# Optimization experiments

Measured on AMD Instinct MI355X. Metric: run time of the kernel, lower is better.

## Reference

```python
import jax, jax.numpy as jnp
import numpy as np

N, E, D, H, L = 100000, 1600000, 128, 64, 3
BN_EPS = 1e-5


def setup_inputs() -> dict:
    key = jax.random.key(0)
    ks = iter(jax.random.split(key, 32))
    r = lambda shape, s=0.05: jax.random.normal(next(ks), shape, dtype=jnp.float32) * s
    inp = {
        "x": jax.random.normal(next(ks), (N, D), dtype=jnp.float32),
        "edge_index": jax.random.randint(next(ks), (2, E), 0, N, dtype=jnp.int64),
        "fa_W1": r((D, H)), "fa_b1": jnp.zeros((H,), jnp.float32),
        "fa_W2": r((H, D)), "fa_b2": jnp.zeros((D,), jnp.float32),
        "proj_W": r((D, H)), "proj_b": jnp.zeros((H,), jnp.float32),
        "gat_W": r((L, H, H)), "gat_asrc": r((L, H)), "gat_adst": r((L, H)),
        "gat_b": jnp.zeros((L, H), jnp.float32),
        "bn_gamma": jnp.ones((L, H), jnp.float32), "bn_beta": jnp.zeros((L, H), jnp.float32),
        "bn_mean": jnp.zeros((L, H), jnp.float32), "bn_var": jnp.ones((L, H), jnp.float32),
        "se_W1": r((3, H // 2)), "se_b1": jnp.zeros((H // 2,), jnp.float32),
        "se_W2": r((H // 2, H)), "se_b2": jnp.zeros((H,), jnp.float32),
        "out_W1": r((2 * H, H)), "out_b1": jnp.zeros((H,), jnp.float32),
        "out_W2": r((H, H // 2)), "out_b2": jnp.zeros((H // 2,), jnp.float32),
        "out_W3": r((H // 2, 1)), "out_b3": jnp.zeros((1,), jnp.float32),
    }
    return inp


def _gat_layer(h, src, dst, n, W, a_src, a_dst, b):
    # PyG GATConv (heads=1, self-loops already appended to src/dst).
    z = h @ W                              # [N,H]
    e = jax.nn.leaky_relu((z @ a_src)[src] + (z @ a_dst)[dst], 0.2)  # [Etot]
    m = jax.ops.segment_max(e, dst, num_segments=n)
    m = jnp.where(jnp.isfinite(m), m, 0.0)
    ex = jnp.exp(e - m[dst])
    denom = jax.ops.segment_sum(ex, dst, num_segments=n)
    alpha = ex / denom[dst]
    return jax.ops.segment_sum(z[src] * alpha[:, None], dst, num_segments=n) + b


def _structural(edge_index, n, dtype):
    src, dst = edge_index[0], edge_index[1]
    deg = jax.ops.segment_sum(jnp.ones(src.shape, dtype), src, num_segments=n)
    norm_deg = deg / jnp.maximum(deg.max(), 1.0)
    infl_sum = jax.ops.segment_sum(deg[dst], src, num_segments=n)
    infl = jnp.where(deg > 0, infl_sum / jnp.maximum(deg, 1.0), 0.0)
    infl = infl / jnp.maximum(infl.max(), 1e-12)
    return jnp.stack([norm_deg, jnp.zeros_like(deg), infl], axis=1)  # [N,3]


def reference(x, edge_index, fa_W1, fa_b1, fa_W2, fa_b2, proj_W, proj_b,
              gat_W, gat_asrc, gat_adst, gat_b, bn_gamma, bn_beta, bn_mean, bn_var,
              se_W1, se_b1, se_W2, se_b2, out_W1, out_b1, out_W2, out_b2, out_W3, out_b3):
    n = x.shape[0]
    # feature attention
    fw = jax.nn.sigmoid(jnp.maximum(x @ fa_W1 + fa_b1, 0.0) @ fa_W2 + fa_b2)
    h = (x * fw) @ proj_W + proj_b
    # self loops for GAT
    loop = jnp.arange(n, dtype=edge_index.dtype)
    src = jnp.concatenate([edge_index[0], loop])
    dst = jnp.concatenate([edge_index[1], loop])
    for l in range(L):
        h = _gat_layer(h, src, dst, n, gat_W[l], gat_asrc[l], gat_adst[l], gat_b[l])
        h = (h - bn_mean[l]) * jax.lax.rsqrt(bn_var[l] + BN_EPS) * bn_gamma[l] + bn_beta[l]
        h = jnp.maximum(h, 0.0)  # eval mode: dropout is identity
    sf = _structural(edge_index, n, h.dtype)
    se = jnp.maximum(sf @ se_W1 + se_b1, 0.0) @ se_W2 + se_b2
    h = jnp.concatenate([h, se], axis=1)  # [N, 2H]
    o = jnp.maximum(h @ out_W1 + out_b1, 0.0)
    o = jnp.maximum(o @ out_W2 + out_b2, 0.0)
    return jax.nn.sigmoid(o @ out_W3 + out_b3)
```

## Files before the change

### kernel.cpp

```cpp
#include <hip/hip_runtime.h>


typedef unsigned int uint;
typedef unsigned short ushort;
typedef __attribute__((ext_vector_type(8))) short bf16x8;
typedef __attribute__((ext_vector_type(4))) float f32x4;

__device__ __forceinline__ uint f2bf(float a) {
    uint u = __float_as_uint(a);
    return (u + 0x7fffu + ((u >> 16) & 1u)) >> 16;
}
__device__ __forceinline__ float bflo(uint p) { return __uint_as_float(p << 16); }
__device__ __forceinline__ float bfhi(uint p) { return __uint_as_float(p & 0xffff0000u); }
__device__ __forceinline__ float b2f16(ushort u) { return __uint_as_float((uint)u << 16); }

__device__ __forceinline__ void packOne(const float* W, int C, int KS,
                                        ushort* dst, int o) {
    int j = o & 7, lane = (o >> 3) & 63, f = o >> 9;
    int ks = f % KS, ct = f / KS;
    int row = 32 * ks + 8 * (lane >> 4) + j;
    int col = ct * 16 + (lane & 15);
    dst[o] = (ushort)f2bf(W[row * C + col]);
}

__global__ void k_pack(const float* __restrict__ faW1, const float* __restrict__ faW2,
                       const float* __restrict__ projW, const float* __restrict__ gatW,
                       const float* __restrict__ oW1, const float* __restrict__ oW2,
                       ushort* __restrict__ pA, ushort* __restrict__ pB,
                       ushort* __restrict__ pC, ushort* __restrict__ pG,
                       ushort* __restrict__ pO1u, ushort* __restrict__ pOW2) {
    int i = blockIdx.x * blockDim.x + threadIdx.x;
    if (i < 8192) packOne(faW1, 64, 4, pA, i);
    else if (i < 16384) packOne(faW2, 128, 2, pB, i - 8192);
    else if (i < 24576) packOne(projW, 64, 4, pC, i - 16384);
    else if (i < 36864) {
        int o = i - 24576; int l = o >> 12;
        packOne(gatW + l * 4096, 64, 2, pG + l * 4096, o & 4095);
    } else if (i < 40960) packOne(oW1, 64, 2, pO1u, i - 36864);
    else if (i < 43008) packOne(oW2, 32, 2, pOW2, i - 40960);
}

__global__ void __launch_bounds__(256)
k_fused1(const float* __restrict__ x,
         const ushort* __restrict__ pA, const float* __restrict__ fab1,
         const ushort* __restrict__ pB, const float* __restrict__ fab2,
         const ushort* __restrict__ pC, const float* __restrict__ projb,
         float* __restrict__ hbuf, int N,
         const int* __restrict__ ei, int E,
         float* __restrict__ deg, int* __restrict__ cursor, int* __restrict__ esrc,
         const float* __restrict__ seW2, const float* __restrict__ seb2,
         const float* __restrict__ oW1, const float* __restrict__ ob1,
         float* __restrict__ M2, float* __restrict__ b2f, ushort* __restrict__ pM2f,
         int gMlp, int gEdge) {
    __shared__ ushort S[4][16][136];
    int bid = blockIdx.x;
    if (bid < gMlp) {
        int wave = threadIdx.x >> 6, lane = threadIdx.x & 63;
        int qg = lane >> 4, lr = lane & 15;
        int n0w = (bid * 4 + wave) * 16;
        int nr = n0w + lr; if (nr >= N) nr = N - 1;
        const float* xr = x + (size_t)nr * 128;
        ushort (*T)[136] = S[wave];
        const bf16x8* fA = reinterpret_cast<const bf16x8*>(pA);
        const bf16x8* fB = reinterpret_cast<const bf16x8*>(pB);
        const bf16x8* fC = reinterpret_cast<const bf16x8*>(pC);

        bf16x8 afr[4];
#pragma unroll
        for (int ks = 0; ks < 4; ++ks) {
            const float* p = xr + 32 * ks + 8 * qg;
            float4 v0 = *reinterpret_cast<const float4*>(p);
            float4 v1 = *reinterpret_cast<const float4*>(p + 4);
            bf16x8 a;
            a[0] = (short)f2bf(v0.x); a[1] = (short)f2bf(v0.y);
            a[2] = (short)f2bf(v0.z); a[3] = (short)f2bf(v0.w);
            a[4] = (short)f2bf(v1.x); a[5] = (short)f2bf(v1.y);
            a[6] = (short)f2bf(v1.z); a[7] = (short)f2bf(v1.w);
            afr[ks] = a;
        }
        {
            f32x4 acc[4] = {{0,0,0,0},{0,0,0,0},{0,0,0,0},{0,0,0,0}};
#pragma unroll
            for (int ct = 0; ct < 4; ++ct)
#pragma unroll
                for (int ks = 0; ks < 4; ++ks)
                    acc[ct] = __builtin_amdgcn_mfma_f32_16x16x32_bf16(
                        afr[ks], fA[(ct * 4 + ks) * 64 + lane], acc[ct], 0, 0, 0);
#pragma unroll
            for (int ct = 0; ct < 4; ++ct) {
                float b1v = fab1[ct * 16 + lr];
#pragma unroll
                for (int r = 0; r < 4; ++r)
                    T[qg * 4 + r][ct * 16 + lr] =
                        (ushort)f2bf(fmaxf(acc[ct][r] + b1v, 0.f));
            }
        }
        __syncthreads();

        bf16x8 bfr[2];
#pragma unroll
        for (int ks = 0; ks < 2; ++ks)
            bfr[ks] = *reinterpret_cast<const bf16x8*>(&T[lr][32 * ks + 8 * qg]);
        __syncthreads();
        {
            f32x4 acc[8] = {{0,0,0,0},{0,0,0,0},{0,0,0,0},{0,0,0,0},
                            {0,0,0,0},{0,0,0,0},{0,0,0,0},{0,0,0,0}};
#pragma unroll
            for (int ct = 0; ct < 8; ++ct)
#pragma unroll
                for (int ks = 0; ks < 2; ++ks)
                    acc[ct] = __builtin_amdgcn_mfma_f32_16x16x32_bf16(
                        bfr[ks], fB[(ct * 2 + ks) * 64 + lane], acc[ct], 0, 0, 0);
#pragma unroll
            for (int ct = 0; ct < 8; ++ct) {
                float b2v = fab2[ct * 16 + lr];
#pragma unroll
                for (int r = 0; r < 4; ++r)
                    T[qg * 4 + r][ct * 16 + lr] = (ushort)f2bf(acc[ct][r] + b2v);
            }
        }
        __syncthreads();

        bf16x8 cfr[4];
#pragma unroll
        for (int ks = 0; ks < 4; ++ks) {
            const ushort* pf = &T[lr][32 * ks + 8 * qg];
            const float* px = xr + 32 * ks + 8 * qg;
            float4 x0 = *reinterpret_cast<const float4*>(px);
            float4 x1 = *reinterpret_cast<const float4*>(px + 4);
            bf16x8 a;
            a[0] = (short)f2bf(x0.x / (1.f + __expf(-b2f16(pf[0]))));
            a[1] = (short)f2bf(x0.y / (1.f + __expf(-b2f16(pf[1]))));
            a[2] = (short)f2bf(x0.z / (1.f + __expf(-b2f16(pf[2]))));
            a[3] = (short)f2bf(x0.w / (1.f + __expf(-b2f16(pf[3]))));
            a[4] = (short)f2bf(x1.x / (1.f + __expf(-b2f16(pf[4]))));
            a[5] = (short)f2bf(x1.y / (1.f + __expf(-b2f16(pf[5]))));
            a[6] = (short)f2bf(x1.z / (1.f + __expf(-b2f16(pf[6]))));
            a[7] = (short)f2bf(x1.w / (1.f + __expf(-b2f16(pf[7]))));
            cfr[ks] = a;
        }
        {
            f32x4 acc[4] = {{0,0,0,0},{0,0,0,0},{0,0,0,0},{0,0,0,0}};
#pragma unroll
            for (int ct = 0; ct < 4; ++ct)
#pragma unroll
                for (int ks = 0; ks < 4; ++ks)
                    acc[ct] = __builtin_amdgcn_mfma_f32_16x16x32_bf16(
                        cfr[ks], fC[(ct * 4 + ks) * 64 + lane], acc[ct], 0, 0, 0);
#pragma unroll
            for (int r = 0; r < 4; ++r) {
                int n = n0w + qg * 4 + r;
                if (n < N) {
#pragma unroll
                    for (int ct = 0; ct < 4; ++ct)
                        hbuf[(size_t)n * 64 + ct * 16 + lr] =
                            acc[ct][r] + projb[ct * 16 + lr];
                    if (lr == 0) esrc[(size_t)n * 64] = n;
                }
            }
        }
    } else if (bid < gMlp + gEdge) {
        int e = (bid - gMlp) * blockDim.x + threadIdx.x;
        if (e < E) {
            int s = ei[e], d = ei[E + e];
            atomicAdd(&deg[s], 1.f);
            int p = atomicAdd(&cursor[d], 1);
            esrc[(size_t)d * 64 + 1 + p] = s;
        }
    } else {
        int tid = threadIdx.x;
        for (int o = tid; o < 32 * 64; o += 256) {
            int k = o >> 6, j = o & 63;
            float s = 0.f;
            for (int i = 0; i < 64; ++i)
                s = fmaf(seW2[k * 64 + i], oW1[(64 + i) * 64 + j], s);
            M2[o] = s;
        }
        for (int j = tid; j < 64; j += 256) {
            float s = ob1[j];
            for (int i = 0; i < 64; ++i)
                s = fmaf(seb2[i], oW1[(64 + i) * 64 + j], s);
            b2f[j] = s;
        }
        __syncthreads();
        for (int o = tid; o < 2048; o += 256)
            packOne(M2, 64, 1, pM2f, o);
    }
}

__global__ __attribute__((amdgpu_waves_per_eu(4, 4))) void __launch_bounds__(256)
k_z(const float* __restrict__ hbuf, const ushort* __restrict__ pWz,
    const float* __restrict__ asrc, const float* __restrict__ adst,
    uint* __restrict__ zbuf, float* __restrict__ es, float* __restrict__ ed,
    const int* __restrict__ ei, int E,
    const float* __restrict__ deg, float* __restrict__ inflsum,
    float* __restrict__ inflv, unsigned* __restrict__ scal,
    int N, int gZ, int riderMode) {
    int bid = blockIdx.x;
    if (bid >= gZ) {
        if (riderMode == 1) {
            int e = (bid - gZ) * blockDim.x + threadIdx.x;
            if (e < E) atomicAdd(&inflsum[ei[e]], deg[ei[E + e]]);
        } else {
            int idx = (bid - gZ) * blockDim.x + threadIdx.x;
            float dv = 0.f, iv = 0.f;
            if (idx < N) {
                dv = deg[idx];
                iv = dv > 0.f ? inflsum[idx] / dv : 0.f;
                inflv[idx] = iv;
            }
            float dm = dv, im = iv;
#pragma unroll
            for (int off = 32; off; off >>= 1) {
                dm = fmaxf(dm, __shfl_xor(dm, off, 64));
                im = fmaxf(im, __shfl_xor(im, off, 64));
            }
            if ((threadIdx.x & 63) == 0) {
                atomicMax(scal + 0, __float_as_uint(dm));
                atomicMax(scal + 1, __float_as_uint(im));
            }
        }
        return;
    }
    __shared__ float zt[4][16][68];
    int wave = threadIdx.x >> 6, lane = threadIdx.x & 63;
    int qg = lane >> 4, lr = lane & 15;
    int n0w = (bid * 4 + wave) * 16;
    int nr = n0w + lr; if (nr >= N) nr = N - 1;

    bf16x8 afr[2];
#pragma unroll
    for (int k2 = 0; k2 < 2; ++k2) {
        const float* hp = hbuf + (size_t)nr * 64 + k2 * 32 + qg * 8;
        float4 h0 = *reinterpret_cast<const float4*>(hp);
        float4 h1 = *reinterpret_cast<const float4*>(hp + 4);
        bf16x8 a;
        a[0] = (short)f2bf(h0.x); a[1] = (short)f2bf(h0.y);
        a[2] = (short)f2bf(h0.z); a[3] = (short)f2bf(h0.w);
        a[4] = (short)f2bf(h1.x); a[5] = (short)f2bf(h1.y);
        a[6] = (short)f2bf(h1.z); a[7] = (short)f2bf(h1.w);
        afr[k2] = a;
    }

    const bf16x8* pw = reinterpret_cast<const bf16x8*>(pWz);
    f32x4 acc0 = {0,0,0,0}, acc1 = {0,0,0,0}, acc2 = {0,0,0,0}, acc3 = {0,0,0,0};
#pragma unroll
    for (int k2 = 0; k2 < 2; ++k2) {
        acc0 = __builtin_amdgcn_mfma_f32_16x16x32_bf16(afr[k2], pw[(0 * 2 + k2) * 64 + lane], acc0, 0, 0, 0);
        acc1 = __builtin_amdgcn_mfma_f32_16x16x32_bf16(afr[k2], pw[(1 * 2 + k2) * 64 + lane], acc1, 0, 0, 0);
        acc2 = __builtin_amdgcn_mfma_f32_16x16x32_bf16(afr[k2], pw[(2 * 2 + k2) * 64 + lane], acc2, 0, 0, 0);
        acc3 = __builtin_amdgcn_mfma_f32_16x16x32_bf16(afr[k2], pw[(3 * 2 + k2) * 64 + lane], acc3, 0, 0, 0);
    }

    float (*Z)[68] = zt[wave];
#pragma unroll
    for (int r = 0; r < 4; ++r) {
        Z[qg * 4 + r][0 * 16 + lr] = acc0[r];
        Z[qg * 4 + r][1 * 16 + lr] = acc1[r];
        Z[qg * 4 + r][2 * 16 + lr] = acc2[r];
        Z[qg * 4 + r][3 * 16 + lr] = acc3[r];
    }
    __syncthreads();

    float zr[16];
    const float* zrow = &Z[lr][qg * 16];
#pragma unroll
    for (int q4 = 0; q4 < 4; ++q4) {
        float4 v = *reinterpret_cast<const float4*>(zrow + q4 * 4);
        zr[q4 * 4] = v.x; zr[q4 * 4 + 1] = v.y; zr[q4 * 4 + 2] = v.z; zr[q4 * 4 + 3] = v.w;
    }
    float pe = 0.f, pd = 0.f;
#pragma unroll
    for (int j = 0; j < 16; ++j) {
        pe = fmaf(zr[j], asrc[qg * 16 + j], pe);
        pd = fmaf(zr[j], adst[qg * 16 + j], pd);
    }
    pe += __shfl_xor(pe, 16, 64); pe += __shfl_xor(pe, 32, 64);
    pd += __shfl_xor(pd, 16, 64); pd += __shfl_xor(pd, 32, 64);

    int n = n0w + lr;
    if (n < N) {
        uint4 u0, u1;
        u0.x = f2bf(zr[0]) | (f2bf(zr[1]) << 16);
        u0.y = f2bf(zr[2]) | (f2bf(zr[3]) << 16);
        u0.z = f2bf(zr[4]) | (f2bf(zr[5]) << 16);
        u0.w = f2bf(zr[6]) | (f2bf(zr[7]) << 16);
        u1.x = f2bf(zr[8]) | (f2bf(zr[9]) << 16);
        u1.y = f2bf(zr[10]) | (f2bf(zr[11]) << 16);
        u1.z = f2bf(zr[12]) | (f2bf(zr[13]) << 16);
        u1.w = f2bf(zr[14]) | (f2bf(zr[15]) << 16);
        uint* zr8 = zbuf + (size_t)n * 32 + qg * 8;
        *reinterpret_cast<uint4*>(zr8) = u0;
        *reinterpret_cast<uint4*>(zr8 + 4) = u1;
        if (qg == 0) { es[n] = pe; ed[n] = pd; }
    }
}

__global__ void k_agg(const int* __restrict__ cursor,
                      const int* __restrict__ esrc,
                      const float* __restrict__ es, const float* __restrict__ ed,
                      const uint* __restrict__ zb,
                      const float* __restrict__ b, const float* __restrict__ g,
                      const float* __restrict__ bta, const float* __restrict__ mean,
                      const float* __restrict__ var,
                      float* __restrict__ hbuf, int N) {
    int wid  = (blockIdx.x * blockDim.x + threadIdx.x) >> 6;
    int lane = threadIdx.x & 63;
    if (wid >= N) return;
    size_t row0 = (size_t)wid * 64;
    int c    = cursor[wid] + 1;
    float edn = ed[wid];
    int lq = lane & 15, q = lane >> 4;

    int   sreg = 0;
    float exv  = 0.f;
    if (lane < c) {
        sreg = esrc[row0 + lane];
        float e = es[sreg] + edn;
        e = e >= 0.f ? e : 0.2f * e;
        exv = __expf(e);
    }
    float ssum = exv;
#pragma unroll
    for (int off = 32; off; off >>= 1) ssum += __shfl_xor(ssum, off, 64);

    float a0 = 0.f, a1 = 0.f, a2 = 0.f, a3 = 0.f;
    for (int e = q; e < c; e += 4) {
        int   se = __shfl(sreg, e, 64);
        float we = __shfl(exv, e, 64);
        uint2 p = *reinterpret_cast<const uint2*>(zb + (size_t)se * 32 + lq * 2);
        a0 = fmaf(bflo(p.x), we, a0);
        a1 = fmaf(bfhi(p.x), we, a1);
        a2 = fmaf(bflo(p.y), we, a2);
        a3 = fmaf(bfhi(p.y), we, a3);
    }
    a0 += __shfl_xor(a0, 16, 64); a0 += __shfl_xor(a0, 32, 64);
    a1 += __shfl_xor(a1, 16, 64); a1 += __shfl_xor(a1, 32, 64);
    a2 += __shfl_xor(a2, 16, 64); a2 += __shfl_xor(a2, 32, 64);
    a3 += __shfl_xor(a3, 16, 64); a3 += __shfl_xor(a3, 32, 64);

    if (q == 0) {
        float inv = 1.f / ssum;
        float4 bb = reinterpret_cast<const float4*>(b)[lq];
        float4 gg = reinterpret_cast<const float4*>(g)[lq];
        float4 tt = reinterpret_cast<const float4*>(bta)[lq];
        float4 mm = reinterpret_cast<const float4*>(mean)[lq];
        float4 vv = reinterpret_cast<const float4*>(var)[lq];
        float v0 = (a0 * inv + bb.x - mm.x) * (gg.x * rsqrtf(vv.x + 1e-5f)) + tt.x;
        float v1 = (a1 * inv + bb.y - mm.y) * (gg.y * rsqrtf(vv.y + 1e-5f)) + tt.y;
        float v2 = (a2 * inv + bb.z - mm.z) * (gg.z * rsqrtf(vv.z + 1e-5f)) + tt.z;
        float v3 = (a3 * inv + bb.w - mm.w) * (gg.w * rsqrtf(vv.w + 1e-5f)) + tt.w;
        reinterpret_cast<float4*>(hbuf + (size_t)wid * 64)[lq] =
            make_float4(fmaxf(v0, 0.f), fmaxf(v1, 0.f), fmaxf(v2, 0.f), fmaxf(v3, 0.f));
    }
}

__global__ void __launch_bounds__(256)
k_final(const float* __restrict__ hbuf, const float* __restrict__ deg,
        const float* __restrict__ inflv, const unsigned* __restrict__ scal,
        const float* __restrict__ seW1, const float* __restrict__ seb1,
        const ushort* __restrict__ pM2f, const float* __restrict__ b2f,
        const ushort* __restrict__ pO1u, const ushort* __restrict__ pOW2,
        const float* __restrict__ ob2,
        const float* __restrict__ oW3, const float* __restrict__ ob3,
        float* __restrict__ out, int N) {
    __shared__ ushort S[4][16][136];
    int wave = threadIdx.x >> 6, lane = threadIdx.x & 63;
    int qg = lane >> 4, lr = lane & 15;
    int n0w = (blockIdx.x * 4 + wave) * 16;
    int nr = n0w + lr; if (nr >= N) nr = N - 1;
    ushort (*T)[136] = S[wave];

    float degmax  = fmaxf(__uint_as_float(scal[0]), 1.0f);
    float inflmax = fmaxf(__uint_as_float(scal[1]), 1e-12f);
    float nd = deg[nr] / degmax;
    float fl = inflv[nr] / inflmax;

    bf16x8 a0, a1, a2;
#pragma unroll
    for (int ks = 0; ks < 2; ++ks) {
        const float* hp = hbuf + (size_t)nr * 64 + 32 * ks + 8 * qg;
        float4 h0 = *reinterpret_cast<const float4*>(hp);
        float4 h1 = *reinterpret_cast<const float4*>(hp + 4);
        bf16x8 a;
        a[0] = (short)f2bf(h0.x); a[1] = (short)f2bf(h0.y);
        a[2] = (short)f2bf(h0.z); a[3] = (short)f2bf(h0.w);
        a[4] = (short)f2bf(h1.x); a[5] = (short)f2bf(h1.y);
        a[6] = (short)f2bf(h1.z); a[7] = (short)f2bf(h1.w);
        if (ks == 0) a0 = a; else a1 = a;
    }
#pragma unroll
    for (int j = 0; j < 8; ++j) {
        int k = 8 * qg + j;
        float hid = fmaxf(fmaf(nd, seW1[k], fmaf(fl, seW1[64 + k], seb1[k])), 0.f);
        a2[j] = (short)f2bf(hid);
    }

    const bf16x8* fO1 = reinterpret_cast<const bf16x8*>(pO1u);
    const bf16x8* fM2 = reinterpret_cast<const bf16x8*>(pM2f);
    const bf16x8* fW2 = reinterpret_cast<const bf16x8*>(pOW2);

    {
        f32x4 acc[4] = {{0,0,0,0},{0,0,0,0},{0,0,0,0},{0,0,0,0}};
#pragma unroll
        for (int ct = 0; ct < 4; ++ct) {
            acc[ct] = __builtin_amdgcn_mfma_f32_16x16x32_bf16(a0, fO1[(ct * 2 + 0) * 64 + lane], acc[ct], 0, 0, 0);
            acc[ct] = __builtin_amdgcn_mfma_f32_16x16x32_bf16(a1, fO1[(ct * 2 + 1) * 64 + lane], acc[ct], 0, 0, 0);
            acc[ct] = __builtin_amdgcn_mfma_f32_16x16x32_bf16(a2, fM2[ct * 64 + lane], acc[ct], 0, 0, 0);
        }
#pragma unroll
        for (int ct = 0; ct < 4; ++ct) {
            float bv = b2f[ct * 16 + lr];
#pragma unroll
            for (int r = 0; r < 4; ++r)
                T[qg * 4 + r][ct * 16 + lr] =
                    (ushort)f2bf(fmaxf(acc[ct][r] + bv, 0.f));
        }
    }
    __syncthreads();

    bf16x8 b0 = *reinterpret_cast<const bf16x8*>(&T[lr][8 * qg]);
    bf16x8 b1 = *reinterpret_cast<const bf16x8*>(&T[lr][32 + 8 * qg]);
    f32x4 o2a = {0,0,0,0}, o2b = {0,0,0,0};
    o2a = __builtin_amdgcn_mfma_f32_16x16x32_bf16(b0, fW2[0 * 64 + lane], o2a, 0, 0, 0);
    o2a = __builtin_amdgcn_mfma_f32_16x16x32_bf16(b1, fW2[1 * 64 + lane], o2a, 0, 0, 0);
    o2b = __builtin_amdgcn_mfma_f32_16x16x32_bf16(b0, fW2[2 * 64 + lane], o2b, 0, 0, 0);
    o2b = __builtin_amdgcn_mfma_f32_16x16x32_bf16(b1, fW2[3 * 64 + lane], o2b, 0, 0, 0);

    float w3a = oW3[lr], w3b = oW3[16 + lr];
    float oba = ob2[lr], obb = ob2[16 + lr];
    float part[4];
#pragma unroll
    for (int r = 0; r < 4; ++r)
        part[r] = fmaxf(o2a[r] + oba, 0.f) * w3a + fmaxf(o2b[r] + obb, 0.f) * w3b;
#pragma unroll
    for (int off = 1; off < 16; off <<= 1) {
#pragma unroll
        for (int r = 0; r < 4; ++r) part[r] += __shfl_xor(part[r], off, 64);
    }
    if (lr == 0) {
        float b3 = ob3[0];
#pragma unroll
        for (int r = 0; r < 4; ++r) {
            int n = n0w + qg * 4 + r;
            if (n < N) out[n] = 1.f / (1.f + __expf(-(part[r] + b3)));
        }
    }
}

extern "C" void kernel_launch(void* const* d_in, const int* in_sizes, int n_in,
                              void* d_out, int out_size, void* d_ws, size_t ws_size,
                              hipStream_t stream) {
    const float* x     = (const float*)d_in[0];
    const int*   ei    = (const int*)d_in[1];
    const float* faW1  = (const float*)d_in[2];
    const float* fab1  = (const float*)d_in[3];
    const float* faW2  = (const float*)d_in[4];
    const float* fab2  = (const float*)d_in[5];
    const float* projW = (const float*)d_in[6];
    const float* projb = (const float*)d_in[7];
    const float* gatW  = (const float*)d_in[8];
    const float* gatAs = (const float*)d_in[9];
    const float* gatAd = (const float*)d_in[10];
    const float* gatB  = (const float*)d_in[11];
    const float* bnG   = (const float*)d_in[12];
    const float* bnB   = (const float*)d_in[13];
    const float* bnM   = (const float*)d_in[14];
    const float* bnV   = (const float*)d_in[15];
    const float* seW1  = (const float*)d_in[16];
    const float* seb1  = (const float*)d_in[17];
    const float* seW2  = (const float*)d_in[18];
    const float* seb2  = (const float*)d_in[19];
    const float* oW1   = (const float*)d_in[20];
    const float* ob1   = (const float*)d_in[21];
    const float* oW2   = (const float*)d_in[22];
    const float* ob2   = (const float*)d_in[23];
    const float* oW3   = (const float*)d_in[24];
    const float* ob3   = (const float*)d_in[25];
    float* out = (float*)d_out;

    const int N = in_sizes[0] / 128;
    const int E = in_sizes[1] / 2;

    float* ws      = (float*)d_ws;
    float* hbuf    = ws;
    uint*  zbuf    = (uint*)(hbuf + (size_t)N * 64);
    float* es      = (float*)(zbuf + (size_t)N * 32);
    float* ed      = es + N;
    float* deg     = ed + N;
    float* inflsum = deg + N;
    unsigned* scal = (unsigned*)(inflsum + N);
    int* cursor    = (int*)(scal + 8);
    float* inflv   = (float*)(cursor + N);
    int* esrc      = (int*)(inflv + N);
    float* M2      = (float*)(esrc + (size_t)N * 64);
    float* b2f     = M2 + 32 * 64;
    ushort* pA   = (ushort*)(b2f + 64);
    ushort* pB   = pA + 8192;
    ushort* pC   = pB + 8192;
    ushort* pWz  = pC + 8192;
    ushort* pO1u = pWz + 3 * 4096;
    ushort* pOW2 = pO1u + 4096;
    ushort* pM2f = pOW2 + 2048;

    dim3 blk(256);
    int gN    = (N + 255) / 256;
    int gE    = (E + 255) / 256;
    int gM    = (N + 63) / 64;
    int blkNW = (N * 64 + 255) / 256;

    hipMemsetAsync(deg, 0, ((size_t)3 * N + 8) * sizeof(float), stream);

    k_pack<<<168, blk, 0, stream>>>(faW1, faW2, projW, gatW, oW1, oW2,
                                    pA, pB, pC, pWz, pO1u, pOW2);

    k_fused1<<<gM + gE + 1, blk, 0, stream>>>(x, pA, fab1, pB, fab2, pC, projb,
                                              hbuf, N, ei, E, deg, cursor, esrc,
                                              seW2, seb2, oW1, ob1, M2, b2f, pM2f,
                                              gM, gE);

    for (int l = 0; l < 3; ++l) {
        int extra = (l == 0) ? gE : (l == 1 ? gN : 0);
        int mode  = (l == 0) ? 1  : (l == 1 ? 2  : 0);
        k_z<<<gM + extra, blk, 0, stream>>>(hbuf, pWz + l * 4096, gatAs + l * 64,
                                            gatAd + l * 64, zbuf, es, ed,
                                            ei, E, deg, inflsum, inflv, scal,
                                            N, gM, mode);
        k_agg<<<blkNW, blk, 0, stream>>>(cursor, esrc, es, ed, zbuf,
                                         gatB + l * 64, bnG + l * 64, bnB + l * 64,
                                         bnM + l * 64, bnV + l * 64, hbuf, N);
    }

    k_final<<<gM, blk, 0, stream>>>(hbuf, deg, inflv, scal, seW1, seb1,
                                    pM2f, b2f, pO1u, pOW2, ob2, oW3, ob3, out, N);
}
```

Measured before the change: 517.1 us.

## Fuse layer-0 GAT projection into input MLP kernel and move influence rider

The first GAT layer's z = h@W plus its attention logits es/ed are now computed directly in the feature-attention/projection kernel, with the projected h staged through shared memory as bf16. This removes one k_z launch and the fp32 hbuf write and read round-trip for layer 0. The edge-influence atomic rider moves from k_z into the layer-0 k_agg launch, and the later k_z calls are shifted to prepare layers 1 and 2. In exchange, h is rounded to bf16 before the GAT matmul, and extra __syncthreads calls are added inside a block whose waves otherwise work independently.

```diff
diff --git a/kernel.cpp b/kernel.cpp
--- a/kernel.cpp
+++ b/kernel.cpp
@@ -45,7 +45,10 @@
          const ushort* __restrict__ pA, const float* __restrict__ fab1,
          const ushort* __restrict__ pB, const float* __restrict__ fab2,
          const ushort* __restrict__ pC, const float* __restrict__ projb,
-         float* __restrict__ hbuf, int N,
+         const ushort* __restrict__ pWz0,
+         const float* __restrict__ asrc, const float* __restrict__ adst,
+         uint* __restrict__ zbuf, float* __restrict__ es, float* __restrict__ ed,
+         int N,
          const int* __restrict__ ei, int E,
          float* __restrict__ deg, int* __restrict__ cursor, int* __restrict__ esrc,
          const float* __restrict__ seW2, const float* __restrict__ seb2,
@@ -64,6 +67,7 @@
         const bf16x8* fA = reinterpret_cast<const bf16x8*>(pA);
         const bf16x8* fB = reinterpret_cast<const bf16x8*>(pB);
         const bf16x8* fC = reinterpret_cast<const bf16x8*>(pC);
+        const bf16x8* fZ = reinterpret_cast<const bf16x8*>(pWz0);
 
         bf16x8 afr[4];
 #pragma unroll
@@ -139,6 +143,7 @@
             a[7] = (short)f2bf(x1.w / (1.f + __expf(-b2f16(pf[7]))));
             cfr[ks] = a;
         }
+        __syncthreads();
         {
             f32x4 acc[4] = {{0,0,0,0},{0,0,0,0},{0,0,0,0},{0,0,0,0}};
 #pragma unroll
@@ -148,15 +153,64 @@
                     acc[ct] = __builtin_amdgcn_mfma_f32_16x16x32_bf16(
                         cfr[ks], fC[(ct * 4 + ks) * 64 + lane], acc[ct], 0, 0, 0);
 #pragma unroll
-            for (int r = 0; r < 4; ++r) {
-                int n = n0w + qg * 4 + r;
-                if (n < N) {
-#pragma unroll
-                    for (int ct = 0; ct < 4; ++ct)
-                        hbuf[(size_t)n * 64 + ct * 16 + lr] =
-                            acc[ct][r] + projb[ct * 16 + lr];
-                    if (lr == 0) esrc[(size_t)n * 64] = n;
-                }
+            for (int ct = 0; ct < 4; ++ct) {
+                float pbv = projb[ct * 16 + lr];
+#pragma unroll
+                for (int r = 0; r < 4; ++r)
+                    T[qg * 4 + r][ct * 16 + lr] = (ushort)f2bf(acc[ct][r] + pbv);
+            }
+        }
+        __syncthreads();
+
+        bf16x8 hfr[2];
+#pragma unroll
+        for (int ks = 0; ks < 2; ++ks)
+            hfr[ks] = *reinterpret_cast<const bf16x8*>(&T[lr][32 * ks + 8 * qg]);
+        __syncthreads();
+        {
+            f32x4 zacc[4] = {{0,0,0,0},{0,0,0,0},{0,0,0,0},{0,0,0,0}};
+#pragma unroll
+            for (int ct = 0; ct < 4; ++ct)
+#pragma unroll
+                for (int ks = 0; ks < 2; ++ks)
+                    zacc[ct] = __builtin_amdgcn_mfma_f32_16x16x32_bf16(
+                        hfr[ks], fZ[(ct * 2 + ks) * 64 + lane], zacc[ct], 0, 0, 0);
+#pragma unroll
+            for (int ct = 0; ct < 4; ++ct)
+#pragma unroll
+                for (int r = 0; r < 4; ++r)
+                    T[qg * 4 + r][ct * 16 + lr] = (ushort)f2bf(zacc[ct][r]);
+        }
+        __syncthreads();
+        {
+            bf16x8 z0 = *reinterpret_cast<const bf16x8*>(&T[lr][qg * 16]);
+            bf16x8 z1 = *reinterpret_cast<const bf16x8*>(&T[lr][qg * 16 + 8]);
+            float pe = 0.f, pd = 0.f;
+#pragma unroll
+            for (int j = 0; j < 8; ++j) {
+                float va = b2f16((ushort)z0[j]), vb = b2f16((ushort)z1[j]);
+                pe = fmaf(va, asrc[qg * 16 + j], pe);
+                pe = fmaf(vb, asrc[qg * 16 + 8 + j], pe);
+                pd = fmaf(va, adst[qg * 16 + j], pd);
+                pd = fmaf(vb, adst[qg * 16 + 8 + j], pd);
+            }
+            pe += __shfl_xor(pe, 16, 64); pe += __shfl_xor(pe, 32, 64);
+            pd += __shfl_xor(pd, 16, 64); pd += __shfl_xor(pd, 32, 64);
+            int n = n0w + lr;
+            if (n < N) {
+                uint4 u0, u1;
+                u0.x = (ushort)z0[0] | ((uint)(ushort)z0[1] << 16);
+                u0.y = (ushort)z0[2] | ((uint)(ushort)z0[3] << 16);
+                u0.z = (ushort)z0[4] | ((uint)(ushort)z0[5] << 16);
+                u0.w = (ushort)z0[6] | ((uint)(ushort)z0[7] << 16);
+                u1.x = (ushort)z1[0] | ((uint)(ushort)z1[1] << 16);
+                u1.y = (ushort)z1[2] | ((uint)(ushort)z1[3] << 16);
+                u1.z = (ushort)z1[4] | ((uint)(ushort)z1[5] << 16);
+                u1.w = (ushort)z1[6] | ((uint)(ushort)z1[7] << 16);
+                uint* zr8 = zbuf + (size_t)n * 32 + qg * 8;
+                *reinterpret_cast<uint4*>(zr8) = u0;
+                *reinterpret_cast<uint4*>(zr8 + 4) = u1;
+                if (qg == 0) { es[n] = pe; ed[n] = pd; esrc[(size_t)n * 64] = n; }
             }
         }
     } else if (bid < gMlp + gEdge) {
@@ -192,33 +246,27 @@
 k_z(const float* __restrict__ hbuf, const ushort* __restrict__ pWz,
     const float* __restrict__ asrc, const float* __restrict__ adst,
     uint* __restrict__ zbuf, float* __restrict__ es, float* __restrict__ ed,
-    const int* __restrict__ ei, int E,
-    const float* __restrict__ deg, float* __restrict__ inflsum,
+    const float* __restrict__ deg, const float* __restrict__ inflsum,
     float* __restrict__ inflv, unsigned* __restrict__ scal,
-    int N, int gZ, int riderMode) {
+    int N, int gZ) {
     int bid = blockIdx.x;
     if (bid >= gZ) {
-        if (riderMode == 1) {
-            int e = (bid - gZ) * blockDim.x + threadIdx.x;
-            if (e < E) atomicAdd(&inflsum[ei[e]], deg[ei[E + e]]);
-        } else {
-            int idx = (bid - gZ) * blockDim.x + threadIdx.x;
-            float dv = 0.f, iv = 0.f;
-            if (idx < N) {
-                dv = deg[idx];
-                iv = dv > 0.f ? inflsum[idx] / dv : 0.f;
-                inflv[idx] = iv;
-            }
-            float dm = dv, im = iv;
-#pragma unroll
-            for (int off = 32; off; off >>= 1) {
-                dm = fmaxf(dm, __shfl_xor(dm, off, 64));
-                im = fmaxf(im, __shfl_xor(im, off, 64));
-            }
-            if ((threadIdx.x & 63) == 0) {
-                atomicMax(scal + 0, __float_as_uint(dm));
-                atomicMax(scal + 1, __float_as_uint(im));
-            }
+        int idx = (bid - gZ) * blockDim.x + threadIdx.x;
+        float dv = 0.f, iv = 0.f;
+        if (idx < N) {
+            dv = deg[idx];
+            iv = dv > 0.f ? inflsum[idx] / dv : 0.f;
+            inflv[idx] = iv;
+        }
+        float dm = dv, im = iv;
+#pragma unroll
+        for (int off = 32; off; off >>= 1) {
+            dm = fmaxf(dm, __shfl_xor(dm, off, 64));
+            im = fmaxf(im, __shfl_xor(im, off, 64));
+        }
+        if ((threadIdx.x & 63) == 0) {
+            atomicMax(scal + 0, __float_as_uint(dm));
+            atomicMax(scal + 1, __float_as_uint(im));
         }
         return;
     }
@@ -303,7 +351,15 @@
                       const float* __restrict__ b, const float* __restrict__ g,
                       const float* __restrict__ bta, const float* __restrict__ mean,
                       const float* __restrict__ var,
-                      float* __restrict__ hbuf, int N) {
+                      float* __restrict__ hbuf, int N,
+                      const int* __restrict__ ei, int E,
+                      const float* __restrict__ deg, float* __restrict__ inflsum,
+                      int gAgg) {
+    if (blockIdx.x >= gAgg) {
+        int e = (blockIdx.x - gAgg) * blockDim.x + threadIdx.x;
+        if (e < E) atomicAdd(&inflsum[ei[e]], deg[ei[E + e]]);
+        return;
+    }
     int wid  = (blockIdx.x * blockDim.x + threadIdx.x) >> 6;
     int lane = threadIdx.x & 63;
     if (wid >= N) return;
@@ -515,20 +571,26 @@
                                     pA, pB, pC, pWz, pO1u, pOW2);
 
     k_fused1<<<gM + gE + 1, blk, 0, stream>>>(x, pA, fab1, pB, fab2, pC, projb,
-                                              hbuf, N, ei, E, deg, cursor, esrc,
+                                              pWz, gatAs, gatAd, zbuf, es, ed, N,
+                                              ei, E, deg, cursor, esrc,
                                               seW2, seb2, oW1, ob1, M2, b2f, pM2f,
                                               gM, gE);
 
     for (int l = 0; l < 3; ++l) {
-        int extra = (l == 0) ? gE : (l == 1 ? gN : 0);
-        int mode  = (l == 0) ? 1  : (l == 1 ? 2  : 0);
-        k_z<<<gM + extra, blk, 0, stream>>>(hbuf, pWz + l * 4096, gatAs + l * 64,
-                                            gatAd + l * 64, zbuf, es, ed,
-                                            ei, E, deg, inflsum, inflv, scal,
-                                            N, gM, mode);
-        k_agg<<<blkNW, blk, 0, stream>>>(cursor, esrc, es, ed, zbuf,
-                                         gatB + l * 64, bnG + l * 64, bnB + l * 64,
-                                         bnM + l * 64, bnV + l * 64, hbuf, N);
+        int aggExtra = (l == 0) ? gE : 0;
+        k_agg<<<blkNW + aggExtra, blk, 0, stream>>>(cursor, esrc, es, ed, zbuf,
+                                                    gatB + l * 64, bnG + l * 64,
+                                                    bnB + l * 64, bnM + l * 64,
+                                                    bnV + l * 64, hbuf, N,
+                                                    ei, E, deg, inflsum, blkNW);
+        if (l < 2) {
+            int extra = (l == 0) ? gN : 0;
+            k_z<<<gM + extra, blk, 0, stream>>>(hbuf, pWz + (l + 1) * 4096,
+                                                gatAs + (l + 1) * 64,
+                                                gatAd + (l + 1) * 64,
+                                                zbuf, es, ed,
+                                                deg, inflsum, inflv, scal, N, gM);
+        }
     }
 
     k_final<<<gM, blk, 0, stream>>>(hbuf, deg, inflv, scal, seW1, seb1,
```

New measurement: 511.5 us, median of 2. Within noise of the previous version (-1.1%).
